# Kernel optimization log

Hardware: AMD Instinct MI355X
Metric: run time of the kernel (lower is better)

Reference implementation:

```python
import jax, jax.numpy as jnp
import numpy as np

HEADS = 2

def gat_layer(x, edge_index, W, att, bias):
    # x: [N, Fin], W: [H*C, Fin], att: [1, H, 2C], bias: [C]
    N = x.shape[0]
    C = bias.shape[0]
    # add self loops (source_to_target: x_j from row 0, aggregate onto row 1)
    loop = jnp.arange(N, dtype=edge_index.dtype)
    src = jnp.concatenate([edge_index[0], loop])
    dst = jnp.concatenate([edge_index[1], loop])
    h = (x @ W.T).reshape(N, HEADS, C)          # [N, H, C]
    x_j = h[src]                                 # [E, H, C]
    x_i = h[dst]                                 # [E, H, C]
    x_cat = jnp.concatenate([x_i, x_j], axis=-1) # [E, H, 2C]
    alpha = (x_cat * att).sum(-1)                # [E, H]
    alpha = jnp.where(alpha >= 0, alpha, 0.2 * alpha)  # leaky_relu(0.2)
    # NOTE: module uses a global (not per-destination) normalization
    alpha = jnp.exp(alpha - alpha.max())
    alpha = alpha / (alpha.sum(axis=0, keepdims=True) + 1e-10)
    msg = x_j * alpha[..., None]                 # [E, H, C]
    aggr = jax.ops.segment_sum(msg, dst, num_segments=N)  # [N, H, C]
    return aggr.mean(axis=1) + bias              # [N, C]

def setup_inputs() -> dict:
    key = jax.random.key(0)
    ks = jax.random.split(key, 7)
    N, Fin, C = 50000, 128, 64
    E = 800000
    x = jax.random.normal(ks[0], (N, Fin), dtype=jnp.float32)
    edge_index = jax.random.randint(ks[1], (2, E), 0, N, dtype=jnp.int64)
    W1 = jax.random.normal(ks[2], (HEADS * C, Fin), dtype=jnp.float32) * 0.05
    att1 = jax.random.normal(ks[3], (1, HEADS, 2 * C), dtype=jnp.float32) * 0.05
    b1 = jnp.zeros((C,), dtype=jnp.float32)
    W2 = jax.random.normal(ks[4], (HEADS * C, C), dtype=jnp.float32) * 0.05
    att2 = jax.random.normal(ks[5], (1, HEADS, 2 * C), dtype=jnp.float32) * 0.05
    b2 = jnp.zeros((C,), dtype=jnp.float32)
    return {"x": x, "edge_index": edge_index, "W1": W1, "att1": att1,
            "b1": b1, "W2": W2, "att2": att2, "b2": b2}

def reference(x, edge_index, W1, att1, b1, W2, att2, b2):
    h = gat_layer(x, edge_index, W1, att1, b1)
    h = jax.nn.relu(h)
    # F.dropout with training flag: treated as eval (identity) for determinism
    out = gat_layer(h, edge_index, W2, att2, b2)
    return out
```

## Files before the change

### kernel.cpp

```cpp
#include <hip/hip_runtime.h>
#include <hip/hip_bf16.h>
#include <math.h>


#define HP 8
#define HG 64
#define NHISTB (HP * HG)
#define HRANGE_MAX 6272
#define NZ    256

using short8 = __attribute__((ext_vector_type(8))) short;
using f32x4  = __attribute__((ext_vector_type(4))) float;

__device__ __forceinline__ unsigned f2bf(float x) {
  unsigned u = __float_as_uint(x);
  return (u + 0x7fffu + ((u >> 16) & 1u)) >> 16;
}
__device__ __forceinline__ float bflo(unsigned p) { return __uint_as_float(p << 16); }
__device__ __forceinline__ float bfhi(unsigned p) { return __uint_as_float(p & 0xffff0000u); }
__device__ __forceinline__ float lrexp(float a) {
  a = a >= 0.f ? a : 0.2f * a;
  return __expf(a);
}

__global__ __launch_bounds__(256) void init_ws(
    const float* __restrict__ W1, const float* __restrict__ W2,
    unsigned short* __restrict__ wbf1, unsigned short* __restrict__ wbf2,
    float* __restrict__ Z) {
  int tid = blockIdx.x * 256 + threadIdx.x;
  int stride = gridDim.x * 256;
  for (int i = tid; i < 128 * 128; i += stride)
    wbf1[i] = (unsigned short)f2bf(W1[i]);
  for (int i = tid; i < 128 * 64; i += stride)
    wbf2[i] = (unsigned short)f2bf(W2[i]);
  if (tid < 4) Z[tid] = 0.f;
}

template <int FIN>
__global__ __launch_bounds__(256) void gemm_mfma(
    const float* __restrict__ x, const unsigned short* __restrict__ Wb,
    const float* __restrict__ att, unsigned* __restrict__ hq,
    float* __restrict__ si, float* __restrict__ sj,
    int N,
    const int* __restrict__ dstE, int* __restrict__ partial,
    int E, int nhistb, int hstep) {
  const int tid = threadIdx.x;

  constexpr int WB = 128 * FIN * 2;
  constexpr int SMEM = (WB > HRANGE_MAX * 4) ? WB : HRANGE_MAX * 4;
  __shared__ __align__(16) unsigned char smem[SMEM];

  if ((int)blockIdx.x < nhistb) {
    int* lhist = (int*)smem;
    const int p = blockIdx.x & (HP - 1);
    const int g = blockIdx.x >> 3;
    const int lo = p * hstep;
    for (int i = tid; i < hstep; i += 256) lhist[i] = 0;
    __syncthreads();
    const int stride = HG * 256;
    int e = g * 256 + tid;
    for (; e + 3 * stride < E; e += 4 * stride) {
      int d0 = dstE[e] - lo;
      int d1 = dstE[e + stride] - lo;
      int d2 = dstE[e + 2 * stride] - lo;
      int d3 = dstE[e + 3 * stride] - lo;
      if ((unsigned)d0 < (unsigned)hstep) atomicAdd(&lhist[d0], 1);
      if ((unsigned)d1 < (unsigned)hstep) atomicAdd(&lhist[d1], 1);
      if ((unsigned)d2 < (unsigned)hstep) atomicAdd(&lhist[d2], 1);
      if ((unsigned)d3 < (unsigned)hstep) atomicAdd(&lhist[d3], 1);
    }
    for (; e < E; e += stride) {
      int d = dstE[e] - lo;
      if ((unsigned)d < (unsigned)hstep) atomicAdd(&lhist[d], 1);
    }
    __syncthreads();
    for (int i = tid; i < hstep; i += 256) {
      int node = lo + i;
      if (node < N) partial[(size_t)g * N + node] = lhist[i];
    }
    return;
  }

  constexpr int KS = FIN / 32;
  constexpr int CPR = FIN / 8;
  constexpr int NCHUNK = 128 * CPR;

  unsigned short* wlds = (unsigned short*)smem;

  const int w    = tid >> 6;
  const int lane = tid & 63;
  const int cl   = lane & 15;
  const int grp  = lane >> 4;
  const int n0   = (blockIdx.x - nhistb) * 64;

  const int arow = n0 + w * 16 + cl;
  const bool avalid = arow < N;
  float4 av0[KS], av1[KS];
#pragma unroll
  for (int ks = 0; ks < KS; ++ks) {
    av0[ks] = make_float4(0.f, 0.f, 0.f, 0.f);
    av1[ks] = av0[ks];
    if (avalid) {
      const float4* xp =
          (const float4*)(x + (size_t)arow * FIN + ks * 32 + grp * 8);
      av0[ks] = xp[0];
      av1[ks] = xp[1];
    }
  }

  const uint4* Wb4 = (const uint4*)Wb;
  for (int c = tid; c < NCHUNK; c += 256) {
    int row = c / CPR;
    int cc  = c & (CPR - 1);
    *(uint4*)&wlds[row * FIN + ((cc ^ (row & (CPR - 1))) * 8)] = Wb4[c];
  }
  __syncthreads();

  short8 afrag[KS];
#pragma unroll
  for (int ks = 0; ks < KS; ++ks) {
    union { short8 s8; unsigned u[4]; } af;
    af.u[0] = f2bf(av0[ks].x) | (f2bf(av0[ks].y) << 16);
    af.u[1] = f2bf(av0[ks].z) | (f2bf(av0[ks].w) << 16);
    af.u[2] = f2bf(av1[ks].x) | (f2bf(av1[ks].y) << 16);
    af.u[3] = f2bf(av1[ks].z) | (f2bf(av1[ks].w) << 16);
    afrag[ks] = af.s8;
  }

  f32x4 acc[8];
#pragma unroll
  for (int ct = 0; ct < 8; ++ct) acc[ct] = (f32x4){0.f, 0.f, 0.f, 0.f};

  const int swz = cl & (CPR - 1);
#pragma unroll
  for (int ks = 0; ks < KS; ++ks) {
#pragma unroll
    for (int ct = 0; ct < 8; ++ct) {
      const unsigned short* bp =
          &wlds[(ct * 16 + cl) * FIN + (((ks * 4 + grp) ^ swz) * 8)];
      short8 bfrag = *(const short8*)bp;
      acc[ct] = __builtin_amdgcn_mfma_f32_16x16x32_bf16(afrag[ks], bfrag,
                                                        acc[ct], 0, 0, 0);
    }
  }

  float ai[8], aj[8];
#pragma unroll
  for (int ct = 0; ct < 8; ++ct) {
    int hd = ct >> 2;
    int cw = (ct & 3) * 16 + cl;
    ai[ct] = att[hd * 128 + cw];
    aj[ct] = att[hd * 128 + 64 + cw];
  }

#pragma unroll
  for (int r = 0; r < 4; ++r) {
    int node = n0 + w * 16 + grp * 4 + r;
    float s0i = 0.f, s0j = 0.f, s1i = 0.f, s1j = 0.f;
    unsigned wpk[4];
#pragma unroll
    for (int ct = 0; ct < 4; ++ct) {
      float v0 = acc[ct][r];
      float v1 = acc[ct + 4][r];
      s0i += v0 * ai[ct];
      s0j += v0 * aj[ct];
      s1i += v1 * ai[ct + 4];
      s1j += v1 * aj[ct + 4];
      wpk[ct] = f2bf(v0) | (f2bf(v1) << 16);
    }
#pragma unroll
    for (int off = 8; off; off >>= 1) {
      s0i += __shfl_xor(s0i, off, 64);
      s0j += __shfl_xor(s0j, off, 64);
      s1i += __shfl_xor(s1i, off, 64);
      s1j += __shfl_xor(s1j, off, 64);
    }
    if (node < N) {
#pragma unroll
      for (int ct = 0; ct < 4; ++ct)
        hq[(size_t)node * 64 + ct * 16 + cl] = wpk[ct];
      if (cl == 0) {
        si[node * 2 + 0] = s0i;
        si[node * 2 + 1] = s1i;
        sj[node * 2 + 0] = s0j;
        sj[node * 2 + 1] = s1j;
      }
    }
  }
}

__device__ __forceinline__ void z_edge_body(
    const int* __restrict__ srcE, const int* __restrict__ dstE,
    const float2* __restrict__ si2, const float2* __restrict__ sj2,
    float* __restrict__ Zp, int E, int Etot, int tid0, int stride) {
  float z0 = 0.f, z1 = 0.f;
  for (int e = tid0; e < Etot; e += stride) {
    int s, d;
    if (e < E) { s = srcE[e]; d = dstE[e]; } else { s = d = e - E; }
    float2 siv = si2[d];
    float2 sjv = sj2[s];
    z0 += lrexp(siv.x + sjv.x);
    z1 += lrexp(siv.y + sjv.y);
  }
  __shared__ float r0[4], r1[4];
  int lane = threadIdx.x & 63, w = threadIdx.x >> 6;
#pragma unroll
  for (int off = 32; off; off >>= 1) {
    z0 += __shfl_down(z0, off, 64);
    z1 += __shfl_down(z1, off, 64);
  }
  if (lane == 0) { r0[w] = z0; r1[w] = z1; }
  __syncthreads();
  if (threadIdx.x == 0) {
    atomicAdd(&Zp[0], r0[0] + r0[1] + r0[2] + r0[3]);
    atomicAdd(&Zp[1], r1[0] + r1[1] + r1[2] + r1[3]);
  }
}

__global__ __launch_bounds__(256) void z_edge(
    const int* __restrict__ srcE, const int* __restrict__ dstE,
    const float2* __restrict__ si2, const float2* __restrict__ sj2,
    float* __restrict__ Zp, int E, int Etot) {
  z_edge_body(srcE, dstE, si2, sj2, Zp, E, Etot,
              blockIdx.x * 256 + threadIdx.x, gridDim.x * 256);
}

__global__ __launch_bounds__(256) void scan_blocks(
    const int* __restrict__ partial, int* __restrict__ rowptr,
    int* __restrict__ bsum, int N) {
  __shared__ int ts[256];
  int b = blockIdx.x, t = threadIdx.x;
  int base = b * 1024 + t * 4;
  int s0 = 0, s1 = 0, s2 = 0, s3 = 0;
  if (base < N) {
    const int4* p4 = (const int4*)partial;
#pragma unroll 4
    for (int g = 0; g < HG; ++g) {
      int4 v = p4[((size_t)g * N + base) >> 2];
      s0 += v.x; s1 += v.y; s2 += v.z; s3 += v.w;
    }
  }
  int v[4] = {s0, s1, s2, s3};
  int tot = s0 + s1 + s2 + s3;
  ts[t] = tot;
  __syncthreads();
#pragma unroll
  for (int off = 1; off < 256; off <<= 1) {
    int x = (t >= off) ? ts[t - off] : 0;
    __syncthreads();
    ts[t] += x;
    __syncthreads();
  }
  int run = ts[t] - tot;
#pragma unroll
  for (int j = 0; j < 4; ++j) {
    if (base + j < N) rowptr[base + j] = run;
    run += v[j];
  }
  if (t == 255) bsum[b] = ts[255];
}

__global__ __launch_bounds__(256) void scan_finish(
    int* __restrict__ rowptr, const int* __restrict__ bsum,
    int* __restrict__ partial, int N, int Eall, int nb) {
  __shared__ int pre[256];
  if (threadIdx.x == 0) {
    int run = 0;
    for (int i = 0; i < nb; ++i) { pre[i] = run; run += bsum[i]; }
  }
  __syncthreads();
  int tid = blockIdx.x * blockDim.x + threadIdx.x;
  int stride = gridDim.x * blockDim.x;
  for (int i = tid; i < N; i += stride) {
    int v = rowptr[i] + pre[i >> 10];
    rowptr[i] = v;
    int run = v;
#pragma unroll 8
    for (int g = 0; g < HG; ++g) {
      int c = partial[(size_t)g * N + i];
      partial[(size_t)g * N + i] = run;
      run += c;
    }
  }
  if (tid == 0) rowptr[N] = Eall;
}

__global__ __launch_bounds__(256) void scatter_z(
    const int* __restrict__ srcE, const int* __restrict__ dstE,
    const int* __restrict__ partial, int* __restrict__ esrc,
    const float2* __restrict__ si2, const float2* __restrict__ sj2,
    float* __restrict__ Zp, int E, int Etot, int hstep, int N) {
  __shared__ __align__(16) int lcur[HRANGE_MAX];
  if ((int)blockIdx.x < NZ) {
    z_edge_body(srcE, dstE, si2, sj2, Zp, E, Etot,
                blockIdx.x * 256 + threadIdx.x, NZ * 256);
    return;
  }
  const int bid = blockIdx.x - NZ;
  const int p = bid & (HP - 1);
  const int g = bid >> 3;
  const int lo = p * hstep;
  const int tid = threadIdx.x;
  for (int i = tid; i < hstep; i += 256) {
    int node = lo + i;
    lcur[i] = (node < N) ? partial[(size_t)g * N + node] : 0;
  }
  __syncthreads();
  const int stride = HG * 256;
  int e = g * 256 + tid;
  for (; e + 3 * stride < E; e += 4 * stride) {
    int d0 = dstE[e] - lo;
    int d1 = dstE[e + stride] - lo;
    int d2 = dstE[e + 2 * stride] - lo;
    int d3 = dstE[e + 3 * stride] - lo;
    if ((unsigned)d0 < (unsigned)hstep) esrc[atomicAdd(&lcur[d0], 1)] = srcE[e];
    if ((unsigned)d1 < (unsigned)hstep) esrc[atomicAdd(&lcur[d1], 1)] = srcE[e + stride];
    if ((unsigned)d2 < (unsigned)hstep) esrc[atomicAdd(&lcur[d2], 1)] = srcE[e + 2 * stride];
    if ((unsigned)d3 < (unsigned)hstep) esrc[atomicAdd(&lcur[d3], 1)] = srcE[e + 3 * stride];
  }
  for (; e < E; e += stride) {
    int d = dstE[e] - lo;
    if ((unsigned)d < (unsigned)hstep) esrc[atomicAdd(&lcur[d], 1)] = srcE[e];
  }
}

__device__ __forceinline__ void edge4(
    const int* __restrict__ esrc, int k, const float2* __restrict__ sj2,
    const unsigned* __restrict__ hq, int lane, float2 siv,
    float& acc0, float& acc1) {
  int s0 = esrc[k], s1 = esrc[k + 1], s2 = esrc[k + 2], s3 = esrc[k + 3];
  float2 j0 = sj2[s0], j1 = sj2[s1], j2 = sj2[s2], j3 = sj2[s3];
  unsigned p0 = hq[(size_t)s0 * 64 + lane];
  unsigned p1 = hq[(size_t)s1 * 64 + lane];
  unsigned p2 = hq[(size_t)s2 * 64 + lane];
  unsigned p3 = hq[(size_t)s3 * 64 + lane];
  acc0 += bflo(p0) * lrexp(siv.x + j0.x) + bflo(p1) * lrexp(siv.x + j1.x) +
          bflo(p2) * lrexp(siv.x + j2.x) + bflo(p3) * lrexp(siv.x + j3.x);
  acc1 += bfhi(p0) * lrexp(siv.y + j0.y) + bfhi(p1) * lrexp(siv.y + j1.y) +
          bfhi(p2) * lrexp(siv.y + j2.y) + bfhi(p3) * lrexp(siv.y + j3.y);
}
__device__ __forceinline__ void edge1(
    int s, const float2* __restrict__ sj2, const unsigned* __restrict__ hq,
    int lane, float2 siv, float& acc0, float& acc1) {
  float2 jv = sj2[s];
  unsigned p = hq[(size_t)s * 64 + lane];
  acc0 += bflo(p) * lrexp(siv.x + jv.x);
  acc1 += bfhi(p) * lrexp(siv.y + jv.y);
}

__global__ __launch_bounds__(256) void csr_aggregate(
    const int* __restrict__ rowptr, const int* __restrict__ esrc,
    const unsigned* __restrict__ hq, const float2* __restrict__ si2,
    const float2* __restrict__ sj2, const float* __restrict__ Zp,
    const float* __restrict__ bias, float* __restrict__ out,
    int N, int do_relu) {
  int lane = threadIdx.x & 63;
  int wid = (blockIdx.x * blockDim.x + threadIdx.x) >> 6;
  int nw = (gridDim.x * blockDim.x) >> 6;
  float z0 = 1.f / (Zp[0] + 1e-10f);
  float z1 = 1.f / (Zp[1] + 1e-10f);
  float bv = bias[lane];
  for (int n0 = wid; n0 < N; n0 += 2 * nw) {
    const int na = __builtin_amdgcn_readfirstlane(n0);
    const bool hasB = (n0 + nw) < N;
    const int nbv = __builtin_amdgcn_readfirstlane(hasB ? n0 + nw : n0);

    int begA = rowptr[na], endA = rowptr[na + 1];
    float2 sivA = si2[na];
    float accA0 = 0.f, accA1 = 0.f;
    edge1(na, sj2, hq, lane, sivA, accA0, accA1);

    int begB = 0, endB = 0;
    float2 sivB = make_float2(0.f, 0.f);
    float accB0 = 0.f, accB1 = 0.f;
    if (hasB) {
      begB = rowptr[nbv];
      endB = rowptr[nbv + 1];
      sivB = si2[nbv];
      edge1(nbv, sj2, hq, lane, sivB, accB0, accB1);
    }

    int ka = begA, kb = begB;
    while (ka + 4 <= endA && kb + 4 <= endB) {
      edge4(esrc, ka, sj2, hq, lane, sivA, accA0, accA1);
      edge4(esrc, kb, sj2, hq, lane, sivB, accB0, accB1);
      ka += 4;
      kb += 4;
    }
    for (; ka + 4 <= endA; ka += 4) edge4(esrc, ka, sj2, hq, lane, sivA, accA0, accA1);
    for (; ka < endA; ++ka) edge1(esrc[ka], sj2, hq, lane, sivA, accA0, accA1);
    for (; kb + 4 <= endB; kb += 4) edge4(esrc, kb, sj2, hq, lane, sivB, accB0, accB1);
    for (; kb < endB; ++kb) edge1(esrc[kb], sj2, hq, lane, sivB, accB0, accB1);

    float rA = 0.5f * (accA0 * z0 + accA1 * z1) + bv;
    if (do_relu) rA = fmaxf(rA, 0.f);
    out[(size_t)na * 64 + lane] = rA;
    if (hasB) {
      float rB = 0.5f * (accB0 * z0 + accB1 * z1) + bv;
      if (do_relu) rB = fmaxf(rB, 0.f);
      out[(size_t)nbv * 64 + lane] = rB;
    }
  }
}

extern "C" void kernel_launch(void* const* d_in, const int* in_sizes, int n_in,
                              void* d_out, int out_size, void* d_ws, size_t ws_size,
                              hipStream_t stream) {
  const float* x    = (const float*)d_in[0];
  const int*   ei   = (const int*)d_in[1];
  const float* W1   = (const float*)d_in[2];
  const float* att1 = (const float*)d_in[3];
  const float* b1   = (const float*)d_in[4];
  const float* W2   = (const float*)d_in[5];
  const float* att2 = (const float*)d_in[6];
  const float* b2   = (const float*)d_in[7];
  float* out = (float*)d_out;

  const int N = in_sizes[0] / 128;
  const int E = in_sizes[1] / 2;
  const int Etot = E + N;
  const int* srcE = ei;
  const int* dstE = ei + E;

  unsigned* hq = (unsigned*)d_ws;
  float* si    = (float*)(hq + (size_t)N * 64);
  float* sj    = si + (size_t)N * 2;
  float* Z     = sj + (size_t)N * 2;
  float* x2    = Z + 4;
  int* partial = (int*)x2;
  int* rowptr  = (int*)(x2 + (size_t)N * 64);
  int* esrc    = rowptr + (N + 1);
  int* bsum    = esrc + E;
  uintptr_t wp = ((uintptr_t)(bsum + 256) + 15) & ~(uintptr_t)15;
  unsigned short* wbf1 = (unsigned short*)wp;
  unsigned short* wbf2 = wbf1 + 128 * 128;

  dim3 blk(256);
  int nb = (N + 1023) / 1024;
  int ntiles = (N + 63) / 64;
  int hstep = (N + HP - 1) / HP;

  init_ws<<<64, blk, 0, stream>>>(W1, W2, wbf1, wbf2, Z);
  gemm_mfma<128><<<NHISTB + ntiles, blk, 0, stream>>>(
      x, wbf1, att1, hq, si, sj, N, dstE, partial, E, NHISTB, hstep);
  scan_blocks<<<nb, blk, 0, stream>>>(partial, rowptr, bsum, N);
  scan_finish<<<256, blk, 0, stream>>>(rowptr, bsum, partial, N, E, nb);
  scatter_z<<<NZ + NHISTB, blk, 0, stream>>>(
      srcE, dstE, partial, esrc, (const float2*)si, (const float2*)sj,
      Z, E, Etot, hstep, N);
  csr_aggregate<<<2048, blk, 0, stream>>>(rowptr, esrc, hq, (const float2*)si,
                                          (const float2*)sj, Z, b1, x2, N, 1);
  gemm_mfma<64><<<ntiles, blk, 0, stream>>>(
      x2, wbf2, att2, hq, si, sj, N, dstE, partial, E, 0, hstep);
  z_edge<<<NZ, blk, 0, stream>>>(srcE, dstE, (const float2*)si,
                                 (const float2*)sj, Z + 2, E, Etot);
  csr_aggregate<<<2048, blk, 0, stream>>>(rowptr, esrc, hq, (const float2*)si,
                                          (const float2*)sj, Z + 2, b2, out, N, 0);
}
```

Measured before the change: 277.9 us.

## Precompute per-edge attention weights in CSR order before aggregation

The scatter step now also records the destination of each CSR edge and computes the exp-leaky-relu attention weights per edge, storing them in a new wgt array. The aggregation kernel reads these precomputed weights instead of gathering sj and computing exp per lane, and drops the two-node interleaving in favour of one node per wave with 4096 blocks. For layer 2, a new wgt_fill kernel recomputes the weights from esrc/edst. This costs extra per-edge writes and reads (edst plus float2 weights), an additional kernel launch, and fewer independent loads in flight per wave.

After: 284.4 us. +2.3%, slower.

```diff
diff --git a/kernel.cpp b/kernel.cpp
--- a/kernel.cpp
+++ b/kernel.cpp
@@ -225,6 +225,19 @@
               blockIdx.x * 256 + threadIdx.x, gridDim.x * 256);
 }
 
+__global__ __launch_bounds__(256) void wgt_fill(
+    const int* __restrict__ esrc, const int* __restrict__ edst,
+    const float2* __restrict__ si2, const float2* __restrict__ sj2,
+    float2* __restrict__ wgt, int E) {
+  int k = blockIdx.x * 256 + threadIdx.x;
+  int stride = gridDim.x * 256;
+  for (; k < E; k += stride) {
+    float2 siv = si2[edst[k]];
+    float2 sjv = sj2[esrc[k]];
+    wgt[k] = make_float2(lrexp(siv.x + sjv.x), lrexp(siv.y + sjv.y));
+  }
+}
+
 __global__ __launch_bounds__(256) void scan_blocks(
     const int* __restrict__ partial, int* __restrict__ rowptr,
     int* __restrict__ bsum, int N) {
@@ -288,6 +301,7 @@
 __global__ __launch_bounds__(256) void scatter_z(
     const int* __restrict__ srcE, const int* __restrict__ dstE,
     const int* __restrict__ partial, int* __restrict__ esrc,
+    int* __restrict__ edst, float2* __restrict__ wgt,
     const float2* __restrict__ si2, const float2* __restrict__ sj2,
     float* __restrict__ Zp, int E, int Etot, int hstep, int N) {
   __shared__ __align__(16) int lcur[HRANGE_MAX];
@@ -307,99 +321,73 @@
   }
   __syncthreads();
   const int stride = HG * 256;
-  int e = g * 256 + tid;
-  for (; e + 3 * stride < E; e += 4 * stride) {
-    int d0 = dstE[e] - lo;
-    int d1 = dstE[e + stride] - lo;
-    int d2 = dstE[e + 2 * stride] - lo;
-    int d3 = dstE[e + 3 * stride] - lo;
-    if ((unsigned)d0 < (unsigned)hstep) esrc[atomicAdd(&lcur[d0], 1)] = srcE[e];
-    if ((unsigned)d1 < (unsigned)hstep) esrc[atomicAdd(&lcur[d1], 1)] = srcE[e + stride];
-    if ((unsigned)d2 < (unsigned)hstep) esrc[atomicAdd(&lcur[d2], 1)] = srcE[e + 2 * stride];
-    if ((unsigned)d3 < (unsigned)hstep) esrc[atomicAdd(&lcur[d3], 1)] = srcE[e + 3 * stride];
-  }
-  for (; e < E; e += stride) {
-    int d = dstE[e] - lo;
-    if ((unsigned)d < (unsigned)hstep) esrc[atomicAdd(&lcur[d], 1)] = srcE[e];
-  }
-}
-
-__device__ __forceinline__ void edge4(
-    const int* __restrict__ esrc, int k, const float2* __restrict__ sj2,
-    const unsigned* __restrict__ hq, int lane, float2 siv,
-    float& acc0, float& acc1) {
+  for (int e = g * 256 + tid; e < E; e += stride) {
+    int d = dstE[e];
+    int dd = d - lo;
+    if ((unsigned)dd < (unsigned)hstep) {
+      int s = srcE[e];
+      int pos = atomicAdd(&lcur[dd], 1);
+      esrc[pos] = s;
+      edst[pos] = d;
+      float2 siv = si2[d];
+      float2 sjv = sj2[s];
+      wgt[pos] = make_float2(lrexp(siv.x + sjv.x), lrexp(siv.y + sjv.y));
+    }
+  }
+}
+
+__device__ __forceinline__ void edge4w(
+    const int* __restrict__ esrc, const float2* __restrict__ wgt, int k,
+    const unsigned* __restrict__ hq, int lane, float& acc0, float& acc1) {
   int s0 = esrc[k], s1 = esrc[k + 1], s2 = esrc[k + 2], s3 = esrc[k + 3];
-  float2 j0 = sj2[s0], j1 = sj2[s1], j2 = sj2[s2], j3 = sj2[s3];
+  float2 w0 = wgt[k], w1 = wgt[k + 1], w2 = wgt[k + 2], w3 = wgt[k + 3];
   unsigned p0 = hq[(size_t)s0 * 64 + lane];
   unsigned p1 = hq[(size_t)s1 * 64 + lane];
   unsigned p2 = hq[(size_t)s2 * 64 + lane];
   unsigned p3 = hq[(size_t)s3 * 64 + lane];
-  acc0 += bflo(p0) * lrexp(siv.x + j0.x) + bflo(p1) * lrexp(siv.x + j1.x) +
-          bflo(p2) * lrexp(siv.x + j2.x) + bflo(p3) * lrexp(siv.x + j3.x);
-  acc1 += bfhi(p0) * lrexp(siv.y + j0.y) + bfhi(p1) * lrexp(siv.y + j1.y) +
-          bfhi(p2) * lrexp(siv.y + j2.y) + bfhi(p3) * lrexp(siv.y + j3.y);
-}
-__device__ __forceinline__ void edge1(
-    int s, const float2* __restrict__ sj2, const unsigned* __restrict__ hq,
-    int lane, float2 siv, float& acc0, float& acc1) {
-  float2 jv = sj2[s];
+  acc0 = fmaf(bflo(p0), w0.x, acc0);
+  acc1 = fmaf(bfhi(p0), w0.y, acc1);
+  acc0 = fmaf(bflo(p1), w1.x, acc0);
+  acc1 = fmaf(bfhi(p1), w1.y, acc1);
+  acc0 = fmaf(bflo(p2), w2.x, acc0);
+  acc1 = fmaf(bfhi(p2), w2.y, acc1);
+  acc0 = fmaf(bflo(p3), w3.x, acc0);
+  acc1 = fmaf(bfhi(p3), w3.y, acc1);
+}
+__device__ __forceinline__ void edge1w(
+    int s, float2 wv, const unsigned* __restrict__ hq, int lane,
+    float& acc0, float& acc1) {
   unsigned p = hq[(size_t)s * 64 + lane];
-  acc0 += bflo(p) * lrexp(siv.x + jv.x);
-  acc1 += bfhi(p) * lrexp(siv.y + jv.y);
+  acc0 = fmaf(bflo(p), wv.x, acc0);
+  acc1 = fmaf(bfhi(p), wv.y, acc1);
 }
 
 __global__ __launch_bounds__(256) void csr_aggregate(
     const int* __restrict__ rowptr, const int* __restrict__ esrc,
-    const unsigned* __restrict__ hq, const float2* __restrict__ si2,
-    const float2* __restrict__ sj2, const float* __restrict__ Zp,
-    const float* __restrict__ bias, float* __restrict__ out,
-    int N, int do_relu) {
+    const float2* __restrict__ wgt, const unsigned* __restrict__ hq,
+    const float2* __restrict__ si2, const float2* __restrict__ sj2,
+    const float* __restrict__ Zp, const float* __restrict__ bias,
+    float* __restrict__ out, int N, int do_relu) {
   int lane = threadIdx.x & 63;
   int wid = (blockIdx.x * blockDim.x + threadIdx.x) >> 6;
   int nw = (gridDim.x * blockDim.x) >> 6;
   float z0 = 1.f / (Zp[0] + 1e-10f);
   float z1 = 1.f / (Zp[1] + 1e-10f);
   float bv = bias[lane];
-  for (int n0 = wid; n0 < N; n0 += 2 * nw) {
-    const int na = __builtin_amdgcn_readfirstlane(n0);
-    const bool hasB = (n0 + nw) < N;
-    const int nbv = __builtin_amdgcn_readfirstlane(hasB ? n0 + nw : n0);
-
-    int begA = rowptr[na], endA = rowptr[na + 1];
-    float2 sivA = si2[na];
-    float accA0 = 0.f, accA1 = 0.f;
-    edge1(na, sj2, hq, lane, sivA, accA0, accA1);
-
-    int begB = 0, endB = 0;
-    float2 sivB = make_float2(0.f, 0.f);
-    float accB0 = 0.f, accB1 = 0.f;
-    if (hasB) {
-      begB = rowptr[nbv];
-      endB = rowptr[nbv + 1];
-      sivB = si2[nbv];
-      edge1(nbv, sj2, hq, lane, sivB, accB0, accB1);
-    }
-
-    int ka = begA, kb = begB;
-    while (ka + 4 <= endA && kb + 4 <= endB) {
-      edge4(esrc, ka, sj2, hq, lane, sivA, accA0, accA1);
-      edge4(esrc, kb, sj2, hq, lane, sivB, accB0, accB1);
-      ka += 4;
-      kb += 4;
-    }
-    for (; ka + 4 <= endA; ka += 4) edge4(esrc, ka, sj2, hq, lane, sivA, accA0, accA1);
-    for (; ka < endA; ++ka) edge1(esrc[ka], sj2, hq, lane, sivA, accA0, accA1);
-    for (; kb + 4 <= endB; kb += 4) edge4(esrc, kb, sj2, hq, lane, sivB, accB0, accB1);
-    for (; kb < endB; ++kb) edge1(esrc[kb], sj2, hq, lane, sivB, accB0, accB1);
-
-    float rA = 0.5f * (accA0 * z0 + accA1 * z1) + bv;
-    if (do_relu) rA = fmaxf(rA, 0.f);
-    out[(size_t)na * 64 + lane] = rA;
-    if (hasB) {
-      float rB = 0.5f * (accB0 * z0 + accB1 * z1) + bv;
-      if (do_relu) rB = fmaxf(rB, 0.f);
-      out[(size_t)nbv * 64 + lane] = rB;
-    }
+  for (int n0 = wid; n0 < N; n0 += nw) {
+    int n = __builtin_amdgcn_readfirstlane(n0);
+    int beg = rowptr[n], end = rowptr[n + 1];
+    float2 siv = si2[n];
+    float2 jv = sj2[n];
+    float2 wself = make_float2(lrexp(siv.x + jv.x), lrexp(siv.y + jv.y));
+    float acc0 = 0.f, acc1 = 0.f;
+    edge1w(n, wself, hq, lane, acc0, acc1);
+    int k = beg;
+    for (; k + 4 <= end; k += 4) edge4w(esrc, wgt, k, hq, lane, acc0, acc1);
+    for (; k < end; ++k) edge1w(esrc[k], wgt[k], hq, lane, acc0, acc1);
+    float r = 0.5f * (acc0 * z0 + acc1 * z1) + bv;
+    if (do_relu) r = fmaxf(r, 0.f);
+    out[(size_t)n * 64 + lane] = r;
   }
 }
 
@@ -430,7 +418,9 @@
   int* partial = (int*)x2;
   int* rowptr  = (int*)(x2 + (size_t)N * 64);
   int* esrc    = rowptr + (N + 1);
-  int* bsum    = esrc + E;
+  int* edst    = esrc + E;
+  float2* wgt  = (float2*)(edst + E);
+  int* bsum    = (int*)(wgt + E);
   uintptr_t wp = ((uintptr_t)(bsum + 256) + 15) & ~(uintptr_t)15;
   unsigned short* wbf1 = (unsigned short*)wp;
   unsigned short* wbf2 = wbf1 + 128 * 128;
@@ -446,14 +436,18 @@
   scan_blocks<<<nb, blk, 0, stream>>>(partial, rowptr, bsum, N);
   scan_finish<<<256, blk, 0, stream>>>(rowptr, bsum, partial, N, E, nb);
   scatter_z<<<NZ + NHISTB, blk, 0, stream>>>(
-      srcE, dstE, partial, esrc, (const float2*)si, (const float2*)sj,
-      Z, E, Etot, hstep, N);
-  csr_aggregate<<<2048, blk, 0, stream>>>(rowptr, esrc, hq, (const float2*)si,
-                                          (const float2*)sj, Z, b1, x2, N, 1);
+      srcE, dstE, partial, esrc, edst, wgt, (const float2*)si,
+      (const float2*)sj, Z, E, Etot, hstep, N);
+  csr_aggregate<<<4096, blk, 0, stream>>>(rowptr, esrc, wgt, hq,
+                                          (const float2*)si, (const float2*)sj,
+                                          Z, b1, x2, N, 1);
   gemm_mfma<64><<<ntiles, blk, 0, stream>>>(
       x2, wbf2, att2, hq, si, sj, N, dstE, partial, E, 0, hstep);
   z_edge<<<NZ, blk, 0, stream>>>(srcE, dstE, (const float2*)si,
                                  (const float2*)sj, Z + 2, E, Etot);
-  csr_aggregate<<<2048, blk, 0, stream>>>(rowptr, esrc, hq, (const float2*)si,
-                                          (const float2*)sj, Z + 2, b2, out, N, 0);
-}
+  wgt_fill<<<512, blk, 0, stream>>>(esrc, edst, (const float2*)si,
+                                    (const float2*)sj, wgt, E);
+  csr_aggregate<<<4096, blk, 0, stream>>>(rowptr, esrc, wgt, hq,
+                                          (const float2*)si, (const float2*)sj,
+                                          Z + 2, b2, out, N, 0);
+}
```
